# Kernel optimization log

Hardware: AMD Instinct MI355X
Metric: run time of the kernel (lower is better)

## Reference

```python
import jax, jax.numpy as jnp
import numpy as np

B, T, N_VARS, VAR_DIM, D = 64, 512, 16, 16, 64
LN_EPS = 1e-3  # Keras LayerNormalization default epsilon


def setup_inputs() -> dict:
    key = jax.random.key(0)
    ks = jax.random.split(key, 20)
    s = 0.02
    return {
        "inputs": jax.random.normal(ks[0], (B, T, N_VARS * VAR_DIM), jnp.float32),
        "context": jax.random.normal(ks[1], (B, D), jnp.float32),
        # per-variable transform Dense
        "Wt": jax.random.normal(ks[2], (N_VARS, VAR_DIM, D), jnp.float32) * s,
        "bt": jnp.zeros((N_VARS, D), jnp.float32),
        # per-variable GRN params
        "Wctx": jax.random.normal(ks[3], (N_VARS, D, D), jnp.float32) * s,  # no bias
        "W1": jax.random.normal(ks[4], (N_VARS, D, D), jnp.float32) * s,
        "b1": jnp.zeros((N_VARS, D), jnp.float32),
        "W2": jax.random.normal(ks[5], (N_VARS, D, D), jnp.float32) * s,
        "b2": jnp.zeros((N_VARS, D), jnp.float32),
        "Wg": jax.random.normal(ks[6], (N_VARS, D, D), jnp.float32) * s,
        "bg": jnp.zeros((N_VARS, D), jnp.float32),
        "Wp": jax.random.normal(ks[7], (N_VARS, D, D), jnp.float32) * s,  # grn_project
        "bp": jnp.zeros((N_VARS, D), jnp.float32),
        "gamma": jnp.ones((N_VARS, D), jnp.float32),
        "beta": jnp.zeros((N_VARS, D), jnp.float32),
        # selection softmax Dense over the flat input
        "Ws": jax.random.normal(ks[8], (N_VARS * VAR_DIM, N_VARS), jnp.float32) * s,
        "bs": jnp.zeros((N_VARS,), jnp.float32),
    }


def _layernorm(x, gamma, beta):
    mu = jnp.mean(x, axis=-1, keepdims=True)
    var = jnp.mean(jnp.square(x - mu), axis=-1, keepdims=True)
    return (x - mu) * jax.lax.rsqrt(var + LN_EPS) * gamma + beta


def reference(inputs, context, Wt, bt, Wctx, W1, b1, W2, b2, Wg, bg, Wp, bp, gamma, beta, Ws, bs):
    # split flat features into variables: [B,T,N,V]
    xv = inputs.reshape(B, T, N_VARS, VAR_DIM)
    # per-variable transform Dense (grouped GEMM): [B,T,N,D]
    t = jnp.einsum('btnv,nvd->btnd', xv, Wt) + bt
    # GRN (inference: dropout inactive)
    residual = jnp.einsum('btnd,nde->btne', t, Wp) + bp
    cproj = jnp.einsum('bd,nde->bne', context, Wctx)  # [B,N,D], broadcast over T
    a = t + cproj[:, None]
    h = jax.nn.elu(jnp.einsum('btnd,nde->btne', a, W1) + b1)
    h = jnp.einsum('btnd,nde->btne', h, W2) + b2
    gate = jax.nn.sigmoid(jnp.einsum('btnd,nde->btne', h, Wg) + bg)
    out = _layernorm(gate * h + residual, gamma, beta)  # [B,T,N,D]
    # selection weights from the flat input
    weights = jax.nn.softmax(jnp.einsum('btf,fn->btn', inputs, Ws) + bs, axis=-1)
    selected = jnp.einsum('btnd,btn->btd', out, weights)
    return selected, weights
```

## Files before the change

### kernel.cpp

```cpp
#include <hip/hip_runtime.h>
#include <math.h>

#define NB 64
#define NT 512
#define NVAR 16
#define VDIM 16
#define DD 64
#define FF 256
#define BT (NB*NT)
#define LN_EPS 1e-3f

typedef __attribute__((ext_vector_type(8))) short bf8;
typedef __attribute__((ext_vector_type(4))) float f4;
typedef __attribute__((ext_vector_type(4))) int i4;
typedef __attribute__((ext_vector_type(4))) unsigned u4;

#define CPROJ_OFF   0
#define RBIAS_OFF   262144
#define WTP_OFF     524288
#define BIGP_OFF    (524288+65536)
#define WSP_OFF     (524288+65536+1048576)

__device__ __forceinline__ void split1(float x, unsigned &hb, float &lo) {
    unsigned u = __builtin_bit_cast(unsigned, x);
    unsigned r = u + 0x7fffu + ((u >> 16) & 1u);
    hb = r >> 16;
    lo = x - __builtin_bit_cast(float, r & 0xffff0000u);
}
__device__ __forceinline__ unsigned rnepk(float x, float y) {
    unsigned a = __builtin_bit_cast(unsigned, x);
    unsigned b = __builtin_bit_cast(unsigned, y);
    a = a + 0x7fffu + ((a >> 16) & 1u);
    b = b + 0x7fffu + ((b >> 16) & 1u);
    return (a >> 16) | (b & 0xffff0000u);
}
__device__ __forceinline__ void split4(f4 v, unsigned &h0, unsigned &h1,
                                       unsigned &l0, unsigned &l1) {
    unsigned b0,b1,b2,b3; float q0,q1,q2,q3;
    split1(v.x,b0,q0); split1(v.y,b1,q1); split1(v.z,b2,q2); split1(v.w,b3,q3);
    h0 = b0 | (b1<<16); h1 = b2 | (b3<<16);
    l0 = rnepk(q0,q1); l1 = rnepk(q2,q3);
}
__device__ __forceinline__ bf8 afrag(u4 w) { return __builtin_bit_cast(bf8, w); }
__device__ __forceinline__ bf8 mk_bhh(unsigned h0, unsigned h1) {
    i4 t; t.x = (int)h0; t.y = (int)h1; t.z = (int)h0; t.w = (int)h1;
    return __builtin_bit_cast(bf8, t);
}
__device__ __forceinline__ bf8 mk_bl0(unsigned l0, unsigned l1) {
    i4 t; t.x = (int)l0; t.y = (int)l1; t.z = 0; t.w = 0;
    return __builtin_bit_cast(bf8, t);
}
__device__ __forceinline__ float bflo(unsigned w){ return __builtin_bit_cast(float, w<<16); }
__device__ __forceinline__ float bfhi(unsigned w){ return __builtin_bit_cast(float, w & 0xffff0000u); }

__device__ __forceinline__ f4 mfma2(f4 acc, bf8 Af, bf8 Bh, bf8 Bl) {
    acc = __builtin_amdgcn_mfma_f32_16x16x32_bf16(Af, Bh, acc, 0,0,0);
    acc = __builtin_amdgcn_mfma_f32_16x16x32_bf16(Af, Bl, acc, 0,0,0);
    return acc;
}

__device__ __forceinline__ void acc_to_frags1(const f4 acc[4],
        unsigned fh[4][2], unsigned fl[4][2]) {
    #pragma unroll
    for (int Ks = 0; Ks < 4; ++Ks)
        split4(acc[Ks], fh[Ks][0], fh[Ks][1], fl[Ks][0], fl[Ks][1]);
}
__device__ __forceinline__ void run_stage2(const u4* __restrict__ ap, int lane,
        const unsigned fh[4][2], const unsigned fl[4][2], f4 acc[4]) {
    #pragma unroll 2
    for (int Ks = 0; Ks < 4; ++Ks) {
        bf8 Bh = mk_bhh(fh[Ks][0], fh[Ks][1]);
        bf8 Bl = mk_bl0(fl[Ks][0], fl[Ks][1]);
        #pragma unroll
        for (int Mi = 0; Mi < 4; ++Mi) {
            u4 w = ap[(Ks*4+Mi)*64 + lane];
            acc[Mi] = mfma2(acc[Mi], afrag(w), Bh, Bl);
        }
    }
}

__global__ void prep_kernel(const float* __restrict__ Wt, const float* __restrict__ W1,
                            const float* __restrict__ W2, const float* __restrict__ Wg,
                            const float* __restrict__ Wp, const float* __restrict__ Ws,
                            const float* __restrict__ ctx, const float* __restrict__ Wctx,
                            u4* __restrict__ wtp, u4* __restrict__ bigp,
                            u4* __restrict__ wsp, float* __restrict__ cproj) {
    if (blockIdx.x >= 276) {
        int bn = (blockIdx.x - 276) * 4 + (threadIdx.x >> 6);
        int b = bn >> 4, n = bn & 15;
        int d = threadIdx.x & 63;
        const float* __restrict__ w = Wctx + n * DD * DD;
        const float* __restrict__ c = ctx + b * DD;
        float acc = 0.f;
        #pragma unroll 8
        for (int k = 0; k < DD; ++k) acc += c[k] * w[k * DD + d];
        cproj[bn * DD + d] = acc;
        return;
    }
    int t = blockIdx.x * 256 + threadIdx.x;
    float v0, v1, v2, v3; u4* dst;
    if (t < 65536) {
        int lane = t & 63, Mi = (t>>6)&3, Ks = (t>>8)&3, mat = (t>>10)&3, var = t>>12;
        const float* W = (mat==0) ? Wp : (mat==1) ? W1 : (mat==2) ? W2 : Wg;
        const float* src = W + var*4096;
        int m = 16*Mi + (lane&15), k0 = 16*Ks + 4*(lane>>4);
        v0 = src[(k0+0)*64+m]; v1 = src[(k0+1)*64+m];
        v2 = src[(k0+2)*64+m]; v3 = src[(k0+3)*64+m];
        dst = bigp + ((var*4+mat)*16 + Ks*4 + Mi)*64 + lane;
    } else if (t < 65536+4096) {
        int r = t - 65536;
        int lane = r & 63, Mi = (r>>6)&3, var = r>>8;
        int m = 16*Mi + (lane&15), k0 = 4*(lane>>4);
        const float* src = Wt + var*1024;
        v0 = src[(k0+0)*64+m]; v1 = src[(k0+1)*64+m];
        v2 = src[(k0+2)*64+m]; v3 = src[(k0+3)*64+m];
        dst = wtp + (var*4+Mi)*64 + lane;
    } else if (t < 65536+4096+1024) {
        int r = t - 69632;
        int lane = r & 63, Ks = r >> 6;
        int m = lane & 15, k0 = 16*Ks + 4*(lane>>4);
        v0 = Ws[(k0+0)*16+m]; v1 = Ws[(k0+1)*16+m];
        v2 = Ws[(k0+2)*16+m]; v3 = Ws[(k0+3)*16+m];
        dst = wsp + Ks*64 + lane;
    } else return;
    f4 v; v.x=v0; v.y=v1; v.z=v2; v.w=v3;
    unsigned h0,h1,l0,l1; split4(v,h0,h1,l0,l1);
    u4 o; o.x=h0; o.y=h1; o.z=l0; o.w=l1;
    *dst = o;
}

__global__ void rbias_kernel(const float* __restrict__ cproj,
                             const float* __restrict__ Wp,
                             const float* __restrict__ bp,
                             float* __restrict__ rbias) {
    int bn = blockIdx.x;
    int n = bn & 15;
    int d = threadIdx.x;
    const float* __restrict__ w = Wp + n * DD * DD;
    const float* __restrict__ c = cproj + bn * DD;
    float acc = bp[n * DD + d];
    #pragma unroll 8
    for (int k = 0; k < DD; ++k) acc -= c[k] * w[k * DD + d];
    rbias[bn * DD + d] = acc;
}

#define PSEL_OFF 0
#define WSEL_OFF 8704
#define SMEM_DW  9792

__global__ __launch_bounds__(512, 4)
void vsn_kernel(const float* __restrict__ inp,
                const u4* __restrict__ wtp, const u4* __restrict__ bigp,
                const u4* __restrict__ wsp,
                const float* __restrict__ bt, const float* __restrict__ b1,
                const float* __restrict__ b2, const float* __restrict__ bg,
                const float* __restrict__ rbias,
                const float* __restrict__ gamma_, const float* __restrict__ beta_,
                const float* __restrict__ bs,
                const float* __restrict__ cproj,
                float* __restrict__ out_sel, float* __restrict__ out_w) {
    __shared__ float smem[SMEM_DW];

    const int tid  = threadIdx.x;
    const int lane = tid & 63;
    const int wv   = tid >> 6;
    const int grp  = wv & 1;
    const int tq   = wv >> 1;
    const int qd   = lane >> 4;
    const int l15  = lane & 15;
    const int tile0 = blockIdx.x * 64;
    const int b     = blockIdx.x >> 3;
    const int tok0  = tile0 + tq * 16;

    const float* row = inp + (size_t)(tok0 + l15) * FF;

    {
        f4 lacc = *(const f4*)(bs + 4*qd);
        #pragma unroll 4
        for (int Ks = 0; Ks < 16; ++Ks) {
            u4 w = wsp[Ks*64 + lane];
            f4 v = *(const f4*)(row + 16*Ks + 4*qd);
            unsigned h0,h1,l0,l1;
            split4(v,h0,h1,l0,l1);
            lacc = mfma2(lacc, afrag(w), mk_bhh(h0,h1), mk_bl0(l0,l1));
        }
        float mx = fmaxf(fmaxf(lacc.x,lacc.y), fmaxf(lacc.z,lacc.w));
        mx = fmaxf(mx, __shfl_xor(mx, 16));
        mx = fmaxf(mx, __shfl_xor(mx, 32));
        float e0 = __expf(lacc.x-mx), e1 = __expf(lacc.y-mx);
        float e2 = __expf(lacc.z-mx), e3 = __expf(lacc.w-mx);
        float s = e0+e1+e2+e3;
        s += __shfl_xor(s, 16);
        s += __shfl_xor(s, 32);
        float rs = 1.f / s;
        e0 *= rs; e1 *= rs; e2 *= rs; e3 *= rs;
        int base = WSEL_OFF + tq*272 + (4*qd)*17 + l15;
        smem[base + 0*17] = e0;
        smem[base + 1*17] = e1;
        smem[base + 2*17] = e2;
        smem[base + 3*17] = e3;
        if (grp == 0) {
            f4 o; o.x=e0; o.y=e1; o.z=e2; o.w=e3;
            *(f4*)(out_w + (size_t)(tok0 + l15)*16 + 4*qd) = o;
        }
    }

    f4 sel[4];
    #pragma unroll
    for (int Mi = 0; Mi < 4; ++Mi) sel[Mi] = (f4)0.f;

    #pragma unroll 1
    for (int vi = 0; vi < 8; ++vi) {
        const int n = grp*8 + vi;
        unsigned fh[4][2], fl[4][2];

        f4 tacc[4];
        #pragma unroll
        for (int Mi = 0; Mi < 4; ++Mi) tacc[Mi] = *(const f4*)(bt + n*DD + 16*Mi + 4*qd);
        {
            f4 v = *(const f4*)(row + n*16 + 4*qd);
            unsigned xh0,xh1,xl0,xl1;
            split4(v, xh0, xh1, xl0, xl1);
            bf8 Bh = mk_bhh(xh0, xh1);
            bf8 Bl = mk_bl0(xl0, xl1);
            #pragma unroll
            for (int Mi = 0; Mi < 4; ++Mi) {
                u4 w = wtp[(n*4+Mi)*64 + lane];
                tacc[Mi] = mfma2(tacc[Mi], afrag(w), Bh, Bl);
            }
        }
        #pragma unroll
        for (int Mi = 0; Mi < 4; ++Mi)
            tacc[Mi] += *(const f4*)(cproj + (size_t)(b*NVAR+n)*DD + 16*Mi + 4*qd);
        acc_to_frags1(tacc, fh, fl);

        f4 racc[4];
        #pragma unroll
        for (int Mi = 0; Mi < 4; ++Mi)
            racc[Mi] = *(const f4*)(rbias + (size_t)(b*NVAR+n)*DD + 16*Mi + 4*qd);
        run_stage2(bigp + (n*4 + 0)*1024, lane, fh, fl, racc);

        f4 hacc[4];
        #pragma unroll
        for (int Mi = 0; Mi < 4; ++Mi) hacc[Mi] = *(const f4*)(b1 + n*DD + 16*Mi + 4*qd);
        run_stage2(bigp + (n*4 + 1)*1024, lane, fh, fl, hacc);
        #pragma unroll
        for (int Mi = 0; Mi < 4; ++Mi) {
            f4& v = hacc[Mi];
            v.x = v.x > 0.f ? v.x : (__expf(v.x)-1.f);
            v.y = v.y > 0.f ? v.y : (__expf(v.y)-1.f);
            v.z = v.z > 0.f ? v.z : (__expf(v.z)-1.f);
            v.w = v.w > 0.f ? v.w : (__expf(v.w)-1.f);
        }
        acc_to_frags1(hacc, fh, fl);

        #pragma unroll
        for (int Mi = 0; Mi < 4; ++Mi) hacc[Mi] = *(const f4*)(b2 + n*DD + 16*Mi + 4*qd);
        run_stage2(bigp + (n*4 + 2)*1024, lane, fh, fl, hacc);
        acc_to_frags1(hacc, fh, fl);

        f4 gacc[4];
        #pragma unroll
        for (int Mi = 0; Mi < 4; ++Mi) gacc[Mi] = *(const f4*)(bg + n*DD + 16*Mi + 4*qd);
        run_stage2(bigp + (n*4 + 3)*1024, lane, fh, fl, gacc);

        f4 z[4];
        #pragma unroll
        for (int Mi = 0; Mi < 4; ++Mi) {
            float h2x = bflo(fh[Mi][0]) + bflo(fl[Mi][0]);
            float h2y = bfhi(fh[Mi][0]) + bfhi(fl[Mi][0]);
            float h2z = bflo(fh[Mi][1]) + bflo(fl[Mi][1]);
            float h2w = bfhi(fh[Mi][1]) + bfhi(fl[Mi][1]);
            f4 gv = gacc[Mi];
            z[Mi].x = h2x / (1.f+__expf(-gv.x)) + racc[Mi].x;
            z[Mi].y = h2y / (1.f+__expf(-gv.y)) + racc[Mi].y;
            z[Mi].z = h2z / (1.f+__expf(-gv.z)) + racc[Mi].z;
            z[Mi].w = h2w / (1.f+__expf(-gv.w)) + racc[Mi].w;
        }
        float s = 0.f;
        #pragma unroll
        for (int Mi = 0; Mi < 4; ++Mi) s += z[Mi].x + z[Mi].y + z[Mi].z + z[Mi].w;
        s += __shfl_xor(s, 16);
        s += __shfl_xor(s, 32);
        float mu = s * (1.f/64.f);
        float q = 0.f;
        #pragma unroll
        for (int Mi = 0; Mi < 4; ++Mi) {
            float dx = z[Mi].x - mu; q += dx*dx;
            dx = z[Mi].y - mu; q += dx*dx;
            dx = z[Mi].z - mu; q += dx*dx;
            dx = z[Mi].w - mu; q += dx*dx;
        }
        q += __shfl_xor(q, 16);
        q += __shfl_xor(q, 32);
        float rstd = rsqrtf(q*(1.f/64.f) + LN_EPS);

        float wn = smem[WSEL_OFF + tq*272 + n*17 + l15];
        #pragma unroll
        for (int Mi = 0; Mi < 4; ++Mi) {
            f4 gm = *(const f4*)(gamma_ + n*DD + 16*Mi + 4*qd);
            f4 bb = *(const f4*)(beta_  + n*DD + 16*Mi + 4*qd);
            sel[Mi].x += wn*((z[Mi].x-mu)*rstd*gm.x + bb.x);
            sel[Mi].y += wn*((z[Mi].y-mu)*rstd*gm.y + bb.y);
            sel[Mi].z += wn*((z[Mi].z-mu)*rstd*gm.z + bb.z);
            sel[Mi].w += wn*((z[Mi].w-mu)*rstd*gm.w + bb.w);
        }
    }

    {
        int base = PSEL_OFF + (grp*64 + tq*16 + l15)*68;
        #pragma unroll
        for (int Mi = 0; Mi < 4; ++Mi)
            *(f4*)&smem[base + 16*Mi + 4*qd] = sel[Mi];
    }
    __syncthreads();
    {
        int tokloc = tid >> 3;
        int d0 = (tid & 7) * 8;
        int rbase = PSEL_OFF + tokloc*68 + d0;
        f4 a0 = *(f4*)&smem[rbase];
        f4 a1 = *(f4*)&smem[rbase + 4];
        f4 b0 = *(f4*)&smem[rbase + 64*68];
        f4 b1v = *(f4*)&smem[rbase + 64*68 + 4];
        float* po = out_sel + (size_t)(tile0+tokloc)*DD + d0;
        *(f4*)po     = a0 + b0;
        *(f4*)(po+4) = a1 + b1v;
    }
}

extern "C" void kernel_launch(void* const* d_in, const int* in_sizes, int n_in,
                              void* d_out, int out_size, void* d_ws, size_t ws_size,
                              hipStream_t stream) {
    const float* inp  = (const float*)d_in[0];
    const float* ctx  = (const float*)d_in[1];
    const float* Wt   = (const float*)d_in[2];
    const float* bt   = (const float*)d_in[3];
    const float* Wctx = (const float*)d_in[4];
    const float* W1   = (const float*)d_in[5];
    const float* b1   = (const float*)d_in[6];
    const float* W2   = (const float*)d_in[7];
    const float* b2   = (const float*)d_in[8];
    const float* Wg   = (const float*)d_in[9];
    const float* bg   = (const float*)d_in[10];
    const float* Wp   = (const float*)d_in[11];
    const float* bp   = (const float*)d_in[12];
    const float* gm   = (const float*)d_in[13];
    const float* bt2  = (const float*)d_in[14];
    const float* Ws   = (const float*)d_in[15];
    const float* bs   = (const float*)d_in[16];

    float* out_sel = (float*)d_out;
    float* out_w   = out_sel + (size_t)BT * DD;

    char* ws = (char*)d_ws;
    float* cproj = (float*)(ws + CPROJ_OFF);
    float* rbias = (float*)(ws + RBIAS_OFF);
    u4* wtp  = (u4*)(ws + WTP_OFF);
    u4* bigp = (u4*)(ws + BIGP_OFF);
    u4* wsp  = (u4*)(ws + WSP_OFF);

    prep_kernel<<<532, 256, 0, stream>>>(Wt, W1, W2, Wg, Wp, Ws, ctx, Wctx,
                                         wtp, bigp, wsp, cproj);
    rbias_kernel<<<NB * NVAR, DD, 0, stream>>>(cproj, Wp, bp, rbias);
    vsn_kernel<<<BT / 64, 512, 0, stream>>>(inp, wtp, bigp, wsp,
                                            bt, b1, b2, bg, rbias, gm, bt2, bs,
                                            cproj, out_sel, out_w);
}
```

Measured before the change: 260.4 us.

## Fuse rbias into prep, truncate low bf16 split, accumulate selection via LDS atomics

Folds the rbias kernel into prep_kernel's context-projection blocks, staging cproj in shared memory and removing one launch. Replaces round-to-nearest packing of the low bf16 residual with plain truncation, making the split cheaper at a small precision cost. Only one wave group computes the selection softmax; the other skips it. The per-thread selection accumulators are replaced by LDS float atomicAdds into a transposed buffer that is zeroed up front, which frees registers but adds atomic traffic and an extra barrier.

```diff
diff --git a/kernel.cpp b/kernel.cpp
--- a/kernel.cpp
+++ b/kernel.cpp
@@ -34,6 +34,11 @@
     b = b + 0x7fffu + ((b >> 16) & 1u);
     return (a >> 16) | (b & 0xffff0000u);
 }
+__device__ __forceinline__ unsigned trpk(float x, float y) {
+    unsigned a = __builtin_bit_cast(unsigned, x);
+    unsigned b = __builtin_bit_cast(unsigned, y);
+    return (a >> 16) | (b & 0xffff0000u);
+}
 __device__ __forceinline__ void split4(f4 v, unsigned &h0, unsigned &h1,
                                        unsigned &l0, unsigned &l1) {
     unsigned b0,b1,b2,b3; float q0,q1,q2,q3;
@@ -41,6 +46,13 @@
     h0 = b0 | (b1<<16); h1 = b2 | (b3<<16);
     l0 = rnepk(q0,q1); l1 = rnepk(q2,q3);
 }
+__device__ __forceinline__ void split4f(f4 v, unsigned &h0, unsigned &h1,
+                                        unsigned &l0, unsigned &l1) {
+    unsigned b0,b1,b2,b3; float q0,q1,q2,q3;
+    split1(v.x,b0,q0); split1(v.y,b1,q1); split1(v.z,b2,q2); split1(v.w,b3,q3);
+    h0 = b0 | (b1<<16); h1 = b2 | (b3<<16);
+    l0 = trpk(q0,q1); l1 = trpk(q2,q3);
+}
 __device__ __forceinline__ bf8 afrag(u4 w) { return __builtin_bit_cast(bf8, w); }
 __device__ __forceinline__ bf8 mk_bhh(unsigned h0, unsigned h1) {
     i4 t; t.x = (int)h0; t.y = (int)h1; t.z = (int)h0; t.w = (int)h1;
@@ -63,7 +75,7 @@
         unsigned fh[4][2], unsigned fl[4][2]) {
     #pragma unroll
     for (int Ks = 0; Ks < 4; ++Ks)
-        split4(acc[Ks], fh[Ks][0], fh[Ks][1], fl[Ks][0], fl[Ks][1]);
+        split4f(acc[Ks], fh[Ks][0], fh[Ks][1], fl[Ks][0], fl[Ks][1]);
 }
 __device__ __forceinline__ void run_stage2(const u4* __restrict__ ap, int lane,
         const unsigned fh[4][2], const unsigned fl[4][2], f4 acc[4]) {
@@ -83,18 +95,28 @@
                             const float* __restrict__ W2, const float* __restrict__ Wg,
                             const float* __restrict__ Wp, const float* __restrict__ Ws,
                             const float* __restrict__ ctx, const float* __restrict__ Wctx,
+                            const float* __restrict__ bp,
                             u4* __restrict__ wtp, u4* __restrict__ bigp,
-                            u4* __restrict__ wsp, float* __restrict__ cproj) {
+                            u4* __restrict__ wsp, float* __restrict__ cproj,
+                            float* __restrict__ rbias) {
     if (blockIdx.x >= 276) {
-        int bn = (blockIdx.x - 276) * 4 + (threadIdx.x >> 6);
+        __shared__ float cp[4][64];
+        int sub = threadIdx.x >> 6, d = threadIdx.x & 63;
+        int bn = (blockIdx.x - 276) * 4 + sub;
         int b = bn >> 4, n = bn & 15;
-        int d = threadIdx.x & 63;
-        const float* __restrict__ w = Wctx + n * DD * DD;
-        const float* __restrict__ c = ctx + b * DD;
+        const float* __restrict__ wc = Wctx + n * DD * DD;
+        const float* __restrict__ c  = ctx + b * DD;
         float acc = 0.f;
         #pragma unroll 8
-        for (int k = 0; k < DD; ++k) acc += c[k] * w[k * DD + d];
+        for (int k = 0; k < DD; ++k) acc += c[k] * wc[k * DD + d];
         cproj[bn * DD + d] = acc;
+        cp[sub][d] = acc;
+        __syncthreads();
+        const float* __restrict__ wp = Wp + n * DD * DD;
+        float r = bp[n * DD + d];
+        #pragma unroll 8
+        for (int k = 0; k < DD; ++k) r -= cp[sub][k] * wp[k * DD + d];
+        rbias[bn * DD + d] = r;
         return;
     }
     int t = blockIdx.x * 256 + threadIdx.x;
@@ -129,21 +151,6 @@
     *dst = o;
 }
 
-__global__ void rbias_kernel(const float* __restrict__ cproj,
-                             const float* __restrict__ Wp,
-                             const float* __restrict__ bp,
-                             float* __restrict__ rbias) {
-    int bn = blockIdx.x;
-    int n = bn & 15;
-    int d = threadIdx.x;
-    const float* __restrict__ w = Wp + n * DD * DD;
-    const float* __restrict__ c = cproj + bn * DD;
-    float acc = bp[n * DD + d];
-    #pragma unroll 8
-    for (int k = 0; k < DD; ++k) acc -= c[k] * w[k * DD + d];
-    rbias[bn * DD + d] = acc;
-}
-
 #define PSEL_OFF 0
 #define WSEL_OFF 8704
 #define SMEM_DW  9792
@@ -174,14 +181,16 @@
 
     const float* row = inp + (size_t)(tok0 + l15) * FF;
 
-    {
+    for (int i = tid; i < 8704; i += 512) smem[PSEL_OFF + i] = 0.f;
+
+    if (grp == 0) {
         f4 lacc = *(const f4*)(bs + 4*qd);
         #pragma unroll 4
         for (int Ks = 0; Ks < 16; ++Ks) {
             u4 w = wsp[Ks*64 + lane];
             f4 v = *(const f4*)(row + 16*Ks + 4*qd);
             unsigned h0,h1,l0,l1;
-            split4(v,h0,h1,l0,l1);
+            split4f(v,h0,h1,l0,l1);
             lacc = mfma2(lacc, afrag(w), mk_bhh(h0,h1), mk_bl0(l0,l1));
         }
         float mx = fmaxf(fmaxf(lacc.x,lacc.y), fmaxf(lacc.z,lacc.w));
@@ -199,15 +208,12 @@
         smem[base + 1*17] = e1;
         smem[base + 2*17] = e2;
         smem[base + 3*17] = e3;
-        if (grp == 0) {
-            f4 o; o.x=e0; o.y=e1; o.z=e2; o.w=e3;
-            *(f4*)(out_w + (size_t)(tok0 + l15)*16 + 4*qd) = o;
-        }
-    }
-
-    f4 sel[4];
-    #pragma unroll
-    for (int Mi = 0; Mi < 4; ++Mi) sel[Mi] = (f4)0.f;
+        f4 o; o.x=e0; o.y=e1; o.z=e2; o.w=e3;
+        *(f4*)(out_w + (size_t)(tok0 + l15)*16 + 4*qd) = o;
+    }
+    __syncthreads();
+
+    const int selbase = PSEL_OFF + grp*4352 + tq*16 + l15;
 
     #pragma unroll 1
     for (int vi = 0; vi < 8; ++vi) {
@@ -220,7 +226,7 @@
         {
             f4 v = *(const f4*)(row + n*16 + 4*qd);
             unsigned xh0,xh1,xl0,xl1;
-            split4(v, xh0, xh1, xl0, xl1);
+            split4f(v, xh0, xh1, xl0, xl1);
             bf8 Bh = mk_bhh(xh0, xh1);
             bf8 Bl = mk_bl0(xl0, xl1);
             #pragma unroll
@@ -300,31 +306,29 @@
         for (int Mi = 0; Mi < 4; ++Mi) {
             f4 gm = *(const f4*)(gamma_ + n*DD + 16*Mi + 4*qd);
             f4 bb = *(const f4*)(beta_  + n*DD + 16*Mi + 4*qd);
-            sel[Mi].x += wn*((z[Mi].x-mu)*rstd*gm.x + bb.x);
-            sel[Mi].y += wn*((z[Mi].y-mu)*rstd*gm.y + bb.y);
-            sel[Mi].z += wn*((z[Mi].z-mu)*rstd*gm.z + bb.z);
-            sel[Mi].w += wn*((z[Mi].w-mu)*rstd*gm.w + bb.w);
-        }
-    }
-
-    {
-        int base = PSEL_OFF + (grp*64 + tq*16 + l15)*68;
-        #pragma unroll
-        for (int Mi = 0; Mi < 4; ++Mi)
-            *(f4*)&smem[base + 16*Mi + 4*qd] = sel[Mi];
-    }
+            int d0 = 16*Mi + 4*qd;
+            atomicAdd(&smem[selbase + (d0+0)*68], wn*((z[Mi].x-mu)*rstd*gm.x + bb.x));
+            atomicAdd(&smem[selbase + (d0+1)*68], wn*((z[Mi].y-mu)*rstd*gm.y + bb.y));
+            atomicAdd(&smem[selbase + (d0+2)*68], wn*((z[Mi].z-mu)*rstd*gm.z + bb.z));
+            atomicAdd(&smem[selbase + (d0+3)*68], wn*((z[Mi].w-mu)*rstd*gm.w + bb.w));
+        }
+    }
+
     __syncthreads();
     {
         int tokloc = tid >> 3;
         int d0 = (tid & 7) * 8;
-        int rbase = PSEL_OFF + tokloc*68 + d0;
-        f4 a0 = *(f4*)&smem[rbase];
-        f4 a1 = *(f4*)&smem[rbase + 4];
-        f4 b0 = *(f4*)&smem[rbase + 64*68];
-        f4 b1v = *(f4*)&smem[rbase + 64*68 + 4];
+        f4 o0, o1;
+        #pragma unroll
+        for (int j = 0; j < 4; ++j) {
+            o0[j] = smem[PSEL_OFF + (d0+j)*68 + tokloc]
+                  + smem[PSEL_OFF + 4352 + (d0+j)*68 + tokloc];
+            o1[j] = smem[PSEL_OFF + (d0+4+j)*68 + tokloc]
+                  + smem[PSEL_OFF + 4352 + (d0+4+j)*68 + tokloc];
+        }
         float* po = out_sel + (size_t)(tile0+tokloc)*DD + d0;
-        *(f4*)po     = a0 + b0;
-        *(f4*)(po+4) = a1 + b1v;
+        *(f4*)po     = o0;
+        *(f4*)(po+4) = o1;
     }
 }
 
@@ -359,9 +363,8 @@
     u4* bigp = (u4*)(ws + BIGP_OFF);
     u4* wsp  = (u4*)(ws + WSP_OFF);
 
-    prep_kernel<<<532, 256, 0, stream>>>(Wt, W1, W2, Wg, Wp, Ws, ctx, Wctx,
-                                         wtp, bigp, wsp, cproj);
-    rbias_kernel<<<NB * NVAR, DD, 0, stream>>>(cproj, Wp, bp, rbias);
+    prep_kernel<<<532, 256, 0, stream>>>(Wt, W1, W2, Wg, Wp, Ws, ctx, Wctx, bp,
+                                         wtp, bigp, wsp, cproj, rbias);
     vsn_kernel<<<BT / 64, 512, 0, stream>>>(inp, wtp, bigp, wsp,
                                             bt, b1, b2, bg, rbias, gm, bt2, bs,
                                             cproj, out_sel, out_w);
```

New measurement: 305.9 us. 17.5% more time.

## Fuse rbias into prep kernel, fold log2e into gate weights, cheapen splits

Applied to the files above, without the earlier changes.

Removes the separate rbias launch by computing rbias inside the cproj blocks of prep_kernel, using shared memory for the context projection. Pre-scales Wg and bg by log2(e) so the sigmoid can use exp2 and a hardware reciprocal instead of expf and a division. Replaces the round-to-nearest bf16 hi/lo split with a truncating split, which is cheaper in ALU ops but loses some precision in the bf16x2 emulation. Also swaps the softmax normalizer divide for rcp.

```diff
diff --git a/kernel.cpp b/kernel.cpp
--- a/kernel.cpp
+++ b/kernel.cpp
@@ -9,6 +9,7 @@
 #define FF 256
 #define BT (NB*NT)
 #define LN_EPS 1e-3f
+#define LOG2E 1.4426950408889634f
 
 typedef __attribute__((ext_vector_type(8))) short bf8;
 typedef __attribute__((ext_vector_type(4))) float f4;
@@ -20,6 +21,7 @@
 #define WTP_OFF     524288
 #define BIGP_OFF    (524288+65536)
 #define WSP_OFF     (524288+65536+1048576)
+#define BGS_OFF     (524288+65536+1048576+16384)
 
 __device__ __forceinline__ void split1(float x, unsigned &hb, float &lo) {
     unsigned u = __builtin_bit_cast(unsigned, x);
@@ -41,6 +43,25 @@
     h0 = b0 | (b1<<16); h1 = b2 | (b3<<16);
     l0 = rnepk(q0,q1); l1 = rnepk(q2,q3);
 }
+__device__ __forceinline__ void split4f(f4 v, unsigned &h0, unsigned &h1,
+                                        unsigned &l0, unsigned &l1) {
+    unsigned a0 = __builtin_bit_cast(unsigned, v.x);
+    unsigned a1 = __builtin_bit_cast(unsigned, v.y);
+    unsigned a2 = __builtin_bit_cast(unsigned, v.z);
+    unsigned a3 = __builtin_bit_cast(unsigned, v.w);
+    unsigned m0 = a0 & 0xffff0000u, m1 = a1 & 0xffff0000u;
+    unsigned m2 = a2 & 0xffff0000u, m3 = a3 & 0xffff0000u;
+    h0 = (a0 >> 16) | m1;
+    h1 = (a2 >> 16) | m3;
+    float lx = v.x - __builtin_bit_cast(float, m0);
+    float ly = v.y - __builtin_bit_cast(float, m1);
+    float lz = v.z - __builtin_bit_cast(float, m2);
+    float lw = v.w - __builtin_bit_cast(float, m3);
+    l0 = (__builtin_bit_cast(unsigned, lx) >> 16) |
+         (__builtin_bit_cast(unsigned, ly) & 0xffff0000u);
+    l1 = (__builtin_bit_cast(unsigned, lz) >> 16) |
+         (__builtin_bit_cast(unsigned, lw) & 0xffff0000u);
+}
 __device__ __forceinline__ bf8 afrag(u4 w) { return __builtin_bit_cast(bf8, w); }
 __device__ __forceinline__ bf8 mk_bhh(unsigned h0, unsigned h1) {
     i4 t; t.x = (int)h0; t.y = (int)h1; t.z = (int)h0; t.w = (int)h1;
@@ -63,7 +84,7 @@
         unsigned fh[4][2], unsigned fl[4][2]) {
     #pragma unroll
     for (int Ks = 0; Ks < 4; ++Ks)
-        split4(acc[Ks], fh[Ks][0], fh[Ks][1], fl[Ks][0], fl[Ks][1]);
+        split4f(acc[Ks], fh[Ks][0], fh[Ks][1], fl[Ks][0], fl[Ks][1]);
 }
 __device__ __forceinline__ void run_stage2(const u4* __restrict__ ap, int lane,
         const unsigned fh[4][2], const unsigned fl[4][2], f4 acc[4]) {
@@ -83,18 +104,28 @@
                             const float* __restrict__ W2, const float* __restrict__ Wg,
                             const float* __restrict__ Wp, const float* __restrict__ Ws,
                             const float* __restrict__ ctx, const float* __restrict__ Wctx,
+                            const float* __restrict__ bp, const float* __restrict__ bg,
                             u4* __restrict__ wtp, u4* __restrict__ bigp,
-                            u4* __restrict__ wsp, float* __restrict__ cproj) {
-    if (blockIdx.x >= 276) {
-        int bn = (blockIdx.x - 276) * 4 + (threadIdx.x >> 6);
+                            u4* __restrict__ wsp, float* __restrict__ cproj,
+                            float* __restrict__ rbias, float* __restrict__ bgs) {
+    if (blockIdx.x >= 280) {
+        __shared__ float cp[4][64];
+        int sub = threadIdx.x >> 6, d = threadIdx.x & 63;
+        int bn = (blockIdx.x - 280) * 4 + sub;
         int b = bn >> 4, n = bn & 15;
-        int d = threadIdx.x & 63;
-        const float* __restrict__ w = Wctx + n * DD * DD;
-        const float* __restrict__ c = ctx + b * DD;
+        const float* __restrict__ wc = Wctx + n * DD * DD;
+        const float* __restrict__ c  = ctx + b * DD;
         float acc = 0.f;
         #pragma unroll 8
-        for (int k = 0; k < DD; ++k) acc += c[k] * w[k * DD + d];
+        for (int k = 0; k < DD; ++k) acc += c[k] * wc[k * DD + d];
         cproj[bn * DD + d] = acc;
+        cp[sub][d] = acc;
+        __syncthreads();
+        const float* __restrict__ wp = Wp + n * DD * DD;
+        float r = bp[n * DD + d];
+        #pragma unroll 8
+        for (int k = 0; k < DD; ++k) r -= cp[sub][k] * wp[k * DD + d];
+        rbias[bn * DD + d] = r;
         return;
     }
     int t = blockIdx.x * 256 + threadIdx.x;
@@ -104,8 +135,9 @@
         const float* W = (mat==0) ? Wp : (mat==1) ? W1 : (mat==2) ? W2 : Wg;
         const float* src = W + var*4096;
         int m = 16*Mi + (lane&15), k0 = 16*Ks + 4*(lane>>4);
-        v0 = src[(k0+0)*64+m]; v1 = src[(k0+1)*64+m];
-        v2 = src[(k0+2)*64+m]; v3 = src[(k0+3)*64+m];
+        float sc = (mat == 3) ? LOG2E : 1.f;
+        v0 = sc*src[(k0+0)*64+m]; v1 = sc*src[(k0+1)*64+m];
+        v2 = sc*src[(k0+2)*64+m]; v3 = sc*src[(k0+3)*64+m];
         dst = bigp + ((var*4+mat)*16 + Ks*4 + Mi)*64 + lane;
     } else if (t < 65536+4096) {
         int r = t - 65536;
@@ -122,6 +154,10 @@
         v0 = Ws[(k0+0)*16+m]; v1 = Ws[(k0+1)*16+m];
         v2 = Ws[(k0+2)*16+m]; v3 = Ws[(k0+3)*16+m];
         dst = wsp + Ks*64 + lane;
+    } else if (t < 65536+4096+1024+1024) {
+        int r = t - 70656;
+        bgs[r] = bg[r] * LOG2E;
+        return;
     } else return;
     f4 v; v.x=v0; v.y=v1; v.z=v2; v.w=v3;
     unsigned h0,h1,l0,l1; split4(v,h0,h1,l0,l1);
@@ -129,21 +165,6 @@
     *dst = o;
 }
 
-__global__ void rbias_kernel(const float* __restrict__ cproj,
-                             const float* __restrict__ Wp,
-                             const float* __restrict__ bp,
-                             float* __restrict__ rbias) {
-    int bn = blockIdx.x;
-    int n = bn & 15;
-    int d = threadIdx.x;
-    const float* __restrict__ w = Wp + n * DD * DD;
-    const float* __restrict__ c = cproj + bn * DD;
-    float acc = bp[n * DD + d];
-    #pragma unroll 8
-    for (int k = 0; k < DD; ++k) acc -= c[k] * w[k * DD + d];
-    rbias[bn * DD + d] = acc;
-}
-
 #define PSEL_OFF 0
 #define WSEL_OFF 8704
 #define SMEM_DW  9792
@@ -153,7 +174,7 @@
                 const u4* __restrict__ wtp, const u4* __restrict__ bigp,
                 const u4* __restrict__ wsp,
                 const float* __restrict__ bt, const float* __restrict__ b1,
-                const float* __restrict__ b2, const float* __restrict__ bg,
+                const float* __restrict__ b2, const float* __restrict__ bgs,
                 const float* __restrict__ rbias,
                 const float* __restrict__ gamma_, const float* __restrict__ beta_,
                 const float* __restrict__ bs,
@@ -181,7 +202,7 @@
             u4 w = wsp[Ks*64 + lane];
             f4 v = *(const f4*)(row + 16*Ks + 4*qd);
             unsigned h0,h1,l0,l1;
-            split4(v,h0,h1,l0,l1);
+            split4f(v,h0,h1,l0,l1);
             lacc = mfma2(lacc, afrag(w), mk_bhh(h0,h1), mk_bl0(l0,l1));
         }
         float mx = fmaxf(fmaxf(lacc.x,lacc.y), fmaxf(lacc.z,lacc.w));
@@ -192,7 +213,7 @@
         float s = e0+e1+e2+e3;
         s += __shfl_xor(s, 16);
         s += __shfl_xor(s, 32);
-        float rs = 1.f / s;
+        float rs = __builtin_amdgcn_rcpf(s);
         e0 *= rs; e1 *= rs; e2 *= rs; e3 *= rs;
         int base = WSEL_OFF + tq*272 + (4*qd)*17 + l15;
         smem[base + 0*17] = e0;
@@ -220,7 +241,7 @@
         {
             f4 v = *(const f4*)(row + n*16 + 4*qd);
             unsigned xh0,xh1,xl0,xl1;
-            split4(v, xh0, xh1, xl0, xl1);
+            split4f(v, xh0, xh1, xl0, xl1);
             bf8 Bh = mk_bhh(xh0, xh1);
             bf8 Bl = mk_bl0(xl0, xl1);
             #pragma unroll
@@ -261,7 +282,7 @@
 
         f4 gacc[4];
         #pragma unroll
-        for (int Mi = 0; Mi < 4; ++Mi) gacc[Mi] = *(const f4*)(bg + n*DD + 16*Mi + 4*qd);
+        for (int Mi = 0; Mi < 4; ++Mi) gacc[Mi] = *(const f4*)(bgs + n*DD + 16*Mi + 4*qd);
         run_stage2(bigp + (n*4 + 3)*1024, lane, fh, fl, gacc);
 
         f4 z[4];
@@ -272,10 +293,10 @@
             float h2z = bflo(fh[Mi][1]) + bflo(fl[Mi][1]);
             float h2w = bfhi(fh[Mi][1]) + bfhi(fl[Mi][1]);
             f4 gv = gacc[Mi];
-            z[Mi].x = h2x / (1.f+__expf(-gv.x)) + racc[Mi].x;
-            z[Mi].y = h2y / (1.f+__expf(-gv.y)) + racc[Mi].y;
-            z[Mi].z = h2z / (1.f+__expf(-gv.z)) + racc[Mi].z;
-            z[Mi].w = h2w / (1.f+__expf(-gv.w)) + racc[Mi].w;
+            z[Mi].x = h2x * __builtin_amdgcn_rcpf(1.f + __builtin_amdgcn_exp2f(-gv.x)) + racc[Mi].x;
+            z[Mi].y = h2y * __builtin_amdgcn_rcpf(1.f + __builtin_amdgcn_exp2f(-gv.y)) + racc[Mi].y;
+            z[Mi].z = h2z * __builtin_amdgcn_rcpf(1.f + __builtin_amdgcn_exp2f(-gv.z)) + racc[Mi].z;
+            z[Mi].w = h2w * __builtin_amdgcn_rcpf(1.f + __builtin_amdgcn_exp2f(-gv.w)) + racc[Mi].w;
         }
         float s = 0.f;
         #pragma unroll
@@ -358,11 +379,11 @@
     u4* wtp  = (u4*)(ws + WTP_OFF);
     u4* bigp = (u4*)(ws + BIGP_OFF);
     u4* wsp  = (u4*)(ws + WSP_OFF);
-
-    prep_kernel<<<532, 256, 0, stream>>>(Wt, W1, W2, Wg, Wp, Ws, ctx, Wctx,
-                                         wtp, bigp, wsp, cproj);
-    rbias_kernel<<<NB * NVAR, DD, 0, stream>>>(cproj, Wp, bp, rbias);
+    float* bgs = (float*)(ws + BGS_OFF);
+
+    prep_kernel<<<536, 256, 0, stream>>>(Wt, W1, W2, Wg, Wp, Ws, ctx, Wctx, bp, bg,
+                                         wtp, bigp, wsp, cproj, rbias, bgs);
     vsn_kernel<<<BT / 64, 512, 0, stream>>>(inp, wtp, bigp, wsp,
-                                            bt, b1, b2, bg, rbias, gm, bt2, bs,
+                                            bt, b1, b2, bgs, rbias, gm, bt2, bs,
                                             cproj, out_sel, out_w);
 }
```

Result: faster. 228.3 us (-12.3%).
